# Kernel optimization log

Hardware: AMD Instinct MI355X
Metric: run time of the kernel (lower is better)

## Reference

```python
import jax, jax.numpy as jnp
import numpy as np

IN_DIM = 128
OUT_DIM = 128
SPLINE_ORDER = 3
GRID_SIZE = 5
NUM_BASIS = GRID_SIZE + SPLINE_ORDER  # 8


def _make_grid():
    # linspace(-1, 1, grid_size+1) extended by spline_order knots on each side
    steps = GRID_SIZE + 1
    g = np.linspace(-1.0, 1.0, steps, dtype=np.float32)
    h = (g[-1] - g[0]) / (steps - 1)
    for _ in range(SPLINE_ORDER):
        g = np.concatenate([[g[0] - h], g, [g[-1] + h]])
    # expand to [in_dim, G]
    return jnp.asarray(np.broadcast_to(g, (IN_DIM, g.shape[0])).copy())


def setup_inputs() -> dict:
    key = jax.random.key(0)
    kx, kc, kw = jax.random.split(key, 3)
    x = jax.random.normal(kx, (8192, IN_DIM), dtype=jnp.float32)
    grid = _make_grid()                                                  # [in, 12]
    spline_coeff = jax.random.normal(kc, (IN_DIM, OUT_DIM, NUM_BASIS), dtype=jnp.float32)
    base_weight = jax.random.normal(kw, (IN_DIM, OUT_DIM), dtype=jnp.float32)
    scale = jnp.ones((1,), dtype=jnp.float32)
    return {"x": x, "grid": grid, "spline_coeff": spline_coeff,
            "base_weight": base_weight, "scale": scale}


def _b_spline_basis(x, grid, order):
    # x: [B, in]; grid: [in, G] -> basis [B, in, G-1-order]
    xg = x[:, :, None]            # [B, in, 1]
    g = grid[None, :, :]          # [1, in, G]
    basis = ((xg >= g[:, :, :-1]) & (xg < g[:, :, 1:])).astype(x.dtype)
    basis = jnp.nan_to_num(basis)
    for k in range(1, order + 1):
        left = (xg - g[:, :, :-(k + 1)]) / (g[:, :, k:-1] - g[:, :, :-(k + 1)]) * basis[:, :, :-1]
        right = (g[:, :, k + 1:] - xg) / (g[:, :, k + 1:] - g[:, :, 1:-k]) * basis[:, :, 1:]
        basis = jnp.nan_to_num(left + right)
    return basis


def reference(x, grid, spline_coeff, base_weight, scale):
    silu = jax.nn.silu(x)                                   # [B, in]
    basis = _b_spline_basis(x, grid, SPLINE_ORDER)          # [B, in, num_basis]
    spline = jnp.einsum('bij,ikj->bik', basis, spline_coeff)  # [B, in, out]
    base = silu[:, :, None] * base_weight[None, :, :]       # [B, in, out]
    y = (base + spline) * scale
    return y.sum(axis=1)                                    # [B, out]
```

## Files before the change

### kernel.cpp

```cpp
#include <hip/hip_runtime.h>
#include <hip/hip_bf16.h>
#include <cstdint>
#include <cstddef>

#define IN_DIM 128
#define OUT_DIM 128
#define NB 8
#define BM 32
#define NT 9
#define A_ROW_BYTES 2304
#define A_BYTES (BM * A_ROW_BYTES)

using bf16 = __hip_bfloat16;
typedef __attribute__((ext_vector_type(8))) short short8;
typedef __attribute__((ext_vector_type(4))) float f32x4;

__device__ __forceinline__ void basis_weights(float xv, float g0, float inv_h,
                                              int& j, float& w0, float& w1,
                                              float& w2, float& w3) {
    float t = (xv - g0) * inv_h;
    float jf = floorf(t);
    j = (int)jf;
    float u = t - jf;
    float um = 1.f - u;
    float u2 = u * u, u3 = u2 * u;
    w0 = um * um * um * (1.f / 6.f);
    w1 = (3.f * u3 - 6.f * u2 + 4.f) * (1.f / 6.f);
    w2 = (-3.f * u3 + 3.f * u2 + 3.f * u + 1.f) * (1.f / 6.f);
    w3 = u3 * (1.f / 6.f);
}

__device__ __forceinline__ unsigned short to_bf16_bits(float v) {
    bf16 h = __float2bfloat16(v);
    return *(unsigned short*)&h;
}

__device__ __forceinline__ short8 pack8(const float4& a, const float4& b) {
    short8 p;
    p[0] = (short)to_bf16_bits(a.x); p[1] = (short)to_bf16_bits(a.y);
    p[2] = (short)to_bf16_bits(a.z); p[3] = (short)to_bf16_bits(a.w);
    p[4] = (short)to_bf16_bits(b.x); p[5] = (short)to_bf16_bits(b.y);
    p[6] = (short)to_bf16_bits(b.z); p[7] = (short)to_bf16_bits(b.w);
    return p;
}

__global__ __launch_bounds__(512)
void k_kan(const float* __restrict__ x, const float* __restrict__ grid,
           const float* __restrict__ C, const float* __restrict__ W,
           const float* __restrict__ scale, float* __restrict__ out) {
    __shared__ __align__(16) char smem[A_BYTES];

    const int tid = threadIdx.x;
    const int lane = tid & 63;
    const int m0 = blockIdx.x * BM;
    const int w = (tid >> 6) & 3;
    const int g = tid >> 8;
    const int r0 = lane & 15;
    const int ksub = lane >> 4;

    int ocol[2];
    ocol[0] = w * 32 + r0;
    ocol[1] = w * 32 + 16 + r0;

    float4 cb[2][2][2];
    float4 pf[2][2][2];

    auto load_spline = [&](int t, float4 (&dst)[2][2][2]) {
#pragma unroll
        for (int k2 = 0; k2 < 2; ++k2) {
            int i = t * 16 + (2 * g + k2) * 4 + ksub;
#pragma unroll
            for (int n = 0; n < 2; ++n) {
                const float* src = C + ((size_t)i * 128 + ocol[n]) * 8;
                dst[k2][n][0] = *(const float4*)src;
                dst[k2][n][1] = *(const float4*)(src + 4);
            }
        }
    };
    auto load_base = [&](float4 (&dst)[2][2][2]) {
#pragma unroll
        for (int k2 = 0; k2 < 2; ++k2) {
            int ibase = (2 * g + k2) * 32 + ksub * 8;
#pragma unroll
            for (int n = 0; n < 2; ++n) {
                float v[8];
#pragma unroll
                for (int e = 0; e < 8; ++e)
                    v[e] = W[(size_t)(ibase + e) * 128 + ocol[n]];
                dst[k2][n][0] = make_float4(v[0], v[1], v[2], v[3]);
                dst[k2][n][1] = make_float4(v[4], v[5], v[6], v[7]);
            }
        }
    };

    load_spline(0, cb);

    {
        int row = tid >> 4, ip = tid & 15;
        const float* xr = x + (size_t)(m0 + row) * IN_DIM + ip * 8;
        float4 xa = *(const float4*)xr;
        float4 xb = *(const float4*)(xr + 4);
        float xv[8] = {xa.x, xa.y, xa.z, xa.w, xb.x, xb.y, xb.z, xb.w};
        float g0 = grid[0];
        float inv_h = 1.f / (grid[4] - grid[3]);
        char* Arow = smem + row * A_ROW_BYTES;
        short8 sil;
#pragma unroll
        for (int e = 0; e < 8; ++e) {
            float v = xv[e];
            sil[e] = (short)to_bf16_bits(v / (1.f + __expf(-v)));
            int j; float w0, w1, w2, w3;
            basis_weights(v, g0, inv_h, j, w0, w1, w2, w3);
            bool inr = (j >= 0) && (j < 11);
            short8 bas;
#pragma unroll
            for (int m = 0; m < 8; ++m) {
                int k2 = m - (j - 3);
                float val = 0.f;
                if (inr && k2 >= 0 && k2 < 4)
                    val = (k2 == 0) ? w0 : (k2 == 1) ? w1 : (k2 == 2) ? w2 : w3;
                bas[m] = (short)to_bf16_bits(val);
            }
            int chunk = (ip * 8 + e) ^ (row & 7);
            *(short8*)(Arow + chunk * 16) = bas;
        }
        int chunk = (128 + ip) ^ (row & 7);
        *(short8*)(Arow + chunk * 16) = sil;
    }
    __syncthreads();

    f32x4 acc[2][2];
#pragma unroll
    for (int rg = 0; rg < 2; ++rg)
#pragma unroll
        for (int n = 0; n < 2; ++n) acc[rg][n] = 0.f;

#pragma unroll
    for (int t = 0; t < NT; ++t) {
        if (t + 1 < 8)        load_spline(t + 1, pf);
        else if (t + 1 == 8)  load_base(pf);

        short8 b[2][2];
#pragma unroll
        for (int k2 = 0; k2 < 2; ++k2)
#pragma unroll
            for (int n = 0; n < 2; ++n)
                b[k2][n] = pack8(cb[k2][n][0], cb[k2][n][1]);

        short8 a[2][2];
#pragma unroll
        for (int rg = 0; rg < 2; ++rg) {
            int row = rg * 16 + r0;
#pragma unroll
            for (int k2 = 0; k2 < 2; ++k2) {
                int c = t * 16 + (2 * g + k2) * 4 + ksub;
                int cs = c ^ (row & 7);
                a[rg][k2] = *(const short8*)(smem + row * A_ROW_BYTES + cs * 16);
            }
        }
#pragma unroll
        for (int k2 = 0; k2 < 2; ++k2)
#pragma unroll
            for (int rg = 0; rg < 2; ++rg)
#pragma unroll
                for (int n = 0; n < 2; ++n)
                    acc[rg][n] = __builtin_amdgcn_mfma_f32_16x16x32_bf16(
                        a[rg][k2], b[k2][n], acc[rg][n], 0, 0, 0);

        if (t + 1 < NT) {
#pragma unroll
            for (int k2 = 0; k2 < 2; ++k2)
#pragma unroll
                for (int n = 0; n < 2; ++n)
#pragma unroll
                    for (int h = 0; h < 2; ++h)
                        cb[k2][n][h] = pf[k2][n][h];
        }
    }

    __syncthreads();
    float* pane = (float*)smem;
    const int pbase = w * (32 * 33);
    if (g == 1) {
#pragma unroll
        for (int rg = 0; rg < 2; ++rg)
#pragma unroll
            for (int n = 0; n < 2; ++n)
#pragma unroll
                for (int q = 0; q < 4; ++q) {
                    int row = rg * 16 + ksub * 4 + q;
                    pane[pbase + row * 33 + n * 16 + r0] = acc[rg][n][q];
                }
    }
    __syncthreads();
    if (g == 0) {
        float s = scale[0];
#pragma unroll
        for (int rg = 0; rg < 2; ++rg)
#pragma unroll
            for (int n = 0; n < 2; ++n)
#pragma unroll
                for (int q = 0; q < 4; ++q) {
                    int row = rg * 16 + ksub * 4 + q;
                    float v = acc[rg][n][q] + pane[pbase + row * 33 + n * 16 + r0];
                    out[(size_t)(m0 + row) * OUT_DIM + w * 32 + n * 16 + r0] = v * s;
                }
    }
}

__global__ void k_naive(const float* __restrict__ x, const float* __restrict__ grid,
                        const float* __restrict__ C, const float* __restrict__ W,
                        const float* __restrict__ scale, float* __restrict__ out) {
    __shared__ float sS[128];
    __shared__ float sB[128][8];
    int b = blockIdx.x, t = threadIdx.x;
    float xv = x[(size_t)b * IN_DIM + t];
    float g0 = grid[0];
    float inv_h = 1.f / (grid[4] - grid[3]);
    sS[t] = xv / (1.f + __expf(-xv));
    int j; float w0, w1, w2, w3;
    basis_weights(xv, g0, inv_h, j, w0, w1, w2, w3);
    bool inrange = (j >= 0) && (j < 11);
#pragma unroll
    for (int m = 0; m < 8; ++m) {
        int k2 = m - (j - 3);
        float val = 0.f;
        if (inrange && k2 >= 0 && k2 < 4)
            val = (k2 == 0) ? w0 : (k2 == 1) ? w1 : (k2 == 2) ? w2 : w3;
        sB[t][m] = val;
    }
    __syncthreads();
    float acc = 0.f;
    for (int i = 0; i < IN_DIM; ++i) {
        acc += sS[i] * W[(size_t)i * OUT_DIM + t];
        const float* c = C + ((size_t)i * OUT_DIM + t) * NB;
#pragma unroll
        for (int m = 0; m < 8; ++m) acc += sB[i][m] * c[m];
    }
    out[(size_t)b * OUT_DIM + t] = acc * scale[0];
}

extern "C" void kernel_launch(void* const* d_in, const int* in_sizes, int n_in,
                              void* d_out, int out_size, void* d_ws, size_t ws_size,
                              hipStream_t stream) {
    const float* x     = (const float*)d_in[0];
    const float* grid  = (const float*)d_in[1];
    const float* C     = (const float*)d_in[2];
    const float* W     = (const float*)d_in[3];
    const float* scale = (const float*)d_in[4];
    float* out = (float*)d_out;

    int B = in_sizes[0] / IN_DIM;

    if ((B % BM) == 0) {
        k_kan<<<B / BM, 512, 0, stream>>>(x, grid, C, W, scale, out);
    } else {
        k_naive<<<B, 128, 0, stream>>>(x, grid, C, W, scale, out);
    }
}
```

Measured before the change: 16.35 us.

## Double row tile to 64 and split K four ways across 16 waves

Doubles the per-block row tile to 64 rows and launches 1024 threads per block. The K dimension is now split four ways: each wave does one k-chunk per step over four row groups. The partial sums of three wave groups go through LDS panes to the first group. The aim is more reuse of each loaded coefficient tile and fewer redundant global loads of C and W across blocks, at the cost of half as many blocks, a larger LDS footprint and a heavier cross-wave reduction.

After: 18.67 us. 14.2% more time.

```diff
diff --git a/kernel.cpp b/kernel.cpp
--- a/kernel.cpp
+++ b/kernel.cpp
@@ -6,7 +6,7 @@
 #define IN_DIM 128
 #define OUT_DIM 128
 #define NB 8
-#define BM 32
+#define BM 64
 #define NT 9
 #define A_ROW_BYTES 2304
 #define A_BYTES (BM * A_ROW_BYTES)
@@ -44,7 +44,7 @@
     return p;
 }
 
-__global__ __launch_bounds__(512)
+__global__ __launch_bounds__(1024)
 void k_kan(const float* __restrict__ x, const float* __restrict__ grid,
            const float* __restrict__ C, const float* __restrict__ W,
            const float* __restrict__ scale, float* __restrict__ out) {
@@ -53,8 +53,9 @@
     const int tid = threadIdx.x;
     const int lane = tid & 63;
     const int m0 = blockIdx.x * BM;
-    const int w = (tid >> 6) & 3;
-    const int g = tid >> 8;
+    const int wave = tid >> 6;
+    const int w = wave & 3;
+    const int g = wave >> 2;
     const int r0 = lane & 15;
     const int ksub = lane >> 4;
 
@@ -62,34 +63,28 @@
     ocol[0] = w * 32 + r0;
     ocol[1] = w * 32 + 16 + r0;
 
-    float4 cb[2][2][2];
-    float4 pf[2][2][2];
-
-    auto load_spline = [&](int t, float4 (&dst)[2][2][2]) {
-#pragma unroll
-        for (int k2 = 0; k2 < 2; ++k2) {
-            int i = t * 16 + (2 * g + k2) * 4 + ksub;
-#pragma unroll
-            for (int n = 0; n < 2; ++n) {
-                const float* src = C + ((size_t)i * 128 + ocol[n]) * 8;
-                dst[k2][n][0] = *(const float4*)src;
-                dst[k2][n][1] = *(const float4*)(src + 4);
-            }
+    float4 cb[2][2];
+    float4 pf[2][2];
+
+    auto load_spline = [&](int t, float4 (&dst)[2][2]) {
+        int i = t * 16 + g * 4 + ksub;
+#pragma unroll
+        for (int n = 0; n < 2; ++n) {
+            const float* src = C + ((size_t)i * 128 + ocol[n]) * 8;
+            dst[n][0] = *(const float4*)src;
+            dst[n][1] = *(const float4*)(src + 4);
         }
     };
-    auto load_base = [&](float4 (&dst)[2][2][2]) {
-#pragma unroll
-        for (int k2 = 0; k2 < 2; ++k2) {
-            int ibase = (2 * g + k2) * 32 + ksub * 8;
-#pragma unroll
-            for (int n = 0; n < 2; ++n) {
-                float v[8];
-#pragma unroll
-                for (int e = 0; e < 8; ++e)
-                    v[e] = W[(size_t)(ibase + e) * 128 + ocol[n]];
-                dst[k2][n][0] = make_float4(v[0], v[1], v[2], v[3]);
-                dst[k2][n][1] = make_float4(v[4], v[5], v[6], v[7]);
-            }
+    auto load_base = [&](float4 (&dst)[2][2]) {
+        int ibase = (g * 4 + ksub) * 8;
+#pragma unroll
+        for (int n = 0; n < 2; ++n) {
+            float v[8];
+#pragma unroll
+            for (int e = 0; e < 8; ++e)
+                v[e] = W[(size_t)(ibase + e) * 128 + ocol[n]];
+            dst[n][0] = make_float4(v[0], v[1], v[2], v[3]);
+            dst[n][1] = make_float4(v[4], v[5], v[6], v[7]);
         }
     };
 
@@ -129,9 +124,9 @@
     }
     __syncthreads();
 
-    f32x4 acc[2][2];
-#pragma unroll
-    for (int rg = 0; rg < 2; ++rg)
+    f32x4 acc[4][2];
+#pragma unroll
+    for (int rg = 0; rg < 4; ++rg)
 #pragma unroll
         for (int n = 0; n < 2; ++n) acc[rg][n] = 0.f;
 
@@ -140,50 +135,41 @@
         if (t + 1 < 8)        load_spline(t + 1, pf);
         else if (t + 1 == 8)  load_base(pf);
 
-        short8 b[2][2];
-#pragma unroll
-        for (int k2 = 0; k2 < 2; ++k2)
-#pragma unroll
-            for (int n = 0; n < 2; ++n)
-                b[k2][n] = pack8(cb[k2][n][0], cb[k2][n][1]);
-
-        short8 a[2][2];
-#pragma unroll
-        for (int rg = 0; rg < 2; ++rg) {
+        short8 b[2];
+#pragma unroll
+        for (int n = 0; n < 2; ++n)
+            b[n] = pack8(cb[n][0], cb[n][1]);
+
+        const int c = t * 16 + g * 4 + ksub;
+        short8 a[4];
+#pragma unroll
+        for (int rg = 0; rg < 4; ++rg) {
             int row = rg * 16 + r0;
-#pragma unroll
-            for (int k2 = 0; k2 < 2; ++k2) {
-                int c = t * 16 + (2 * g + k2) * 4 + ksub;
-                int cs = c ^ (row & 7);
-                a[rg][k2] = *(const short8*)(smem + row * A_ROW_BYTES + cs * 16);
-            }
-        }
-#pragma unroll
-        for (int k2 = 0; k2 < 2; ++k2)
-#pragma unroll
-            for (int rg = 0; rg < 2; ++rg)
-#pragma unroll
-                for (int n = 0; n < 2; ++n)
-                    acc[rg][n] = __builtin_amdgcn_mfma_f32_16x16x32_bf16(
-                        a[rg][k2], b[k2][n], acc[rg][n], 0, 0, 0);
+            int cs = c ^ (row & 7);
+            a[rg] = *(const short8*)(smem + row * A_ROW_BYTES + cs * 16);
+        }
+#pragma unroll
+        for (int rg = 0; rg < 4; ++rg)
+#pragma unroll
+            for (int n = 0; n < 2; ++n)
+                acc[rg][n] = __builtin_amdgcn_mfma_f32_16x16x32_bf16(
+                    a[rg], b[n], acc[rg][n], 0, 0, 0);
 
         if (t + 1 < NT) {
 #pragma unroll
-            for (int k2 = 0; k2 < 2; ++k2)
-#pragma unroll
-                for (int n = 0; n < 2; ++n)
-#pragma unroll
-                    for (int h = 0; h < 2; ++h)
-                        cb[k2][n][h] = pf[k2][n][h];
+            for (int n = 0; n < 2; ++n)
+#pragma unroll
+                for (int h = 0; h < 2; ++h)
+                    cb[n][h] = pf[n][h];
         }
     }
 
     __syncthreads();
     float* pane = (float*)smem;
-    const int pbase = w * (32 * 33);
-    if (g == 1) {
-#pragma unroll
-        for (int rg = 0; rg < 2; ++rg)
+    if (g > 0) {
+        const int pbase = (w * 3 + (g - 1)) * (64 * 33);
+#pragma unroll
+        for (int rg = 0; rg < 4; ++rg)
 #pragma unroll
             for (int n = 0; n < 2; ++n)
 #pragma unroll
@@ -195,14 +181,18 @@
     __syncthreads();
     if (g == 0) {
         float s = scale[0];
-#pragma unroll
-        for (int rg = 0; rg < 2; ++rg)
+        const int pb0 = (w * 3 + 0) * (64 * 33);
+        const int pb1 = (w * 3 + 1) * (64 * 33);
+        const int pb2 = (w * 3 + 2) * (64 * 33);
+#pragma unroll
+        for (int rg = 0; rg < 4; ++rg)
 #pragma unroll
             for (int n = 0; n < 2; ++n)
 #pragma unroll
                 for (int q = 0; q < 4; ++q) {
                     int row = rg * 16 + ksub * 4 + q;
-                    float v = acc[rg][n][q] + pane[pbase + row * 33 + n * 16 + r0];
+                    int po = row * 33 + n * 16 + r0;
+                    float v = acc[rg][n][q] + pane[pb0 + po] + pane[pb1 + po] + pane[pb2 + po];
                     out[(size_t)(m0 + row) * OUT_DIM + w * 32 + n * 16 + r0] = v * s;
                 }
     }
@@ -253,7 +243,7 @@
     int B = in_sizes[0] / IN_DIM;
 
     if ((B % BM) == 0) {
-        k_kan<<<B / BM, 512, 0, stream>>>(x, grid, C, W, scale, out);
+        k_kan<<<B / BM, 1024, 0, stream>>>(x, grid, C, W, scale, out);
     } else {
         k_naive<<<B, 128, 0, stream>>>(x, grid, C, W, scale, out);
     }
```
